# Optimization experiments

Measured on AMD Instinct MI355X. Metric: run time of the kernel, lower is better.

Reference implementation:

```python
import jax, jax.numpy as jnp
import numpy as np

TOP_K = 2


def setup_inputs() -> dict:
    key = jax.random.key(0)
    ks = jax.random.split(key, 6)
    B, S, H, I, E = 2, 1024, 1024, 2048, 8
    s_h = 1.0 / np.sqrt(H)
    s_i = 1.0 / np.sqrt(I)
    return {
        "x": jax.random.normal(ks[0], (B, S, H), jnp.float32),
        "gate_w": jax.random.normal(ks[1], (H, E), jnp.float32) * s_h,
        "gate_b": jnp.zeros((E,), jnp.float32),
        "w1": jax.random.normal(ks[2], (E, H, I), jnp.float32) * s_h,
        "w3": jax.random.normal(ks[3], (E, H, I), jnp.float32) * s_h,
        "w2": jax.random.normal(ks[4], (E, I, H), jnp.float32) * s_i,
    }


def reference(x, gate_w, gate_b, w1, w3, w2):
    # Gating: softmax over experts, then top-k selection + renormalization.
    logits = jnp.einsum("bsh,he->bse", x, gate_w) + gate_b            # [B,S,E]
    probs = jax.nn.softmax(logits, axis=-1)
    topk_w, topk_idx = jax.lax.top_k(probs, TOP_K)                    # [B,S,K]
    topk_w = topk_w / jnp.sum(topk_w, axis=-1, keepdims=True)

    E = gate_w.shape[-1]
    # Per-token combine weight for each expert (0 if not routed there).
    # one_hot: [B,S,K,E] -> combine: [B,S,E]
    combine = jnp.sum(jax.nn.one_hot(topk_idx, E, dtype=x.dtype) * topk_w[..., None], axis=-2)

    # SwiGLU expert FFN: down(silu(gate(x)) * up(x)); dense-masked reference
    # (compute every expert on every token, weight by combine; math identical
    # to the original gather/scatter loop since combine is 0 off-route).
    out = jnp.zeros_like(x)
    for e in range(E):
        h = jax.nn.silu(x @ w1[e]) * (x @ w3[e])                      # [B,S,I]
        out = out + combine[..., e:e + 1] * (h @ w2[e])               # [B,S,H]
    return out
```

## Files before the change

### kernel.cpp

```cpp
#include <hip/hip_runtime.h>
#include <hip/hip_bf16.h>
#include <math.h>

typedef __attribute__((ext_vector_type(4))) float f32x4;
typedef __attribute__((ext_vector_type(8))) short bf16x8;

#define T_TOK 2048
#define H_DIM 1024
#define I_DIM 2048
#define E_NUM 8

__device__ inline unsigned short f2bf(float f) {
  union { float f; unsigned int u; } v; v.f = f;
  unsigned int r = v.u + 0x7fffu + ((v.u >> 16) & 1u);
  return (unsigned short)(r >> 16);
}
__device__ inline unsigned int pack2(float a, float b) {
  return (unsigned int)f2bf(a) | ((unsigned int)f2bf(b) << 16);
}

__device__ inline void gld16(const void* g, void* l) {
  __builtin_amdgcn_global_load_lds((const __attribute__((address_space(1))) void*)g,
                                   (__attribute__((address_space(3))) void*)l, 16, 0, 0);
}

__device__ inline void transpose_tile(const float* __restrict__ ip, unsigned short* __restrict__ op,
                                      int R, int C, int rt, int ct, char* smem)
{
  unsigned short (*tl)[66] = (unsigned short (*)[66])smem;
  int r0 = rt * 64, c0 = ct * 64;
  int tid = threadIdx.x;
  int rq = (tid >> 4) * 4;
  int c4 = (tid & 15) * 4;
  const float* base = ip + (size_t)(r0 + rq) * C + c0 + c4;
  float4 v0 = *(const float4*)(base);
  float4 v1 = *(const float4*)(base + C);
  float4 v2 = *(const float4*)(base + 2 * C);
  float4 v3 = *(const float4*)(base + 3 * C);
  const float* f0 = (const float*)&v0;
  const float* f1 = (const float*)&v1;
  const float* f2 = (const float*)&v2;
  const float* f3 = (const float*)&v3;
#pragma unroll
  for (int j = 0; j < 4; ++j) {
    *(unsigned int*)&tl[c4 + j][rq]     = pack2(f0[j], f1[j]);
    *(unsigned int*)&tl[c4 + j][rq + 2] = pack2(f2[j], f3[j]);
  }
  __syncthreads();
  int c = tid >> 3, r8 = (tid & 7) * 8;
#pragma unroll
  for (int it = 0; it < 2; ++it) {
    int cc = c + it * 32;
    uint4 o;
    o.x = *(const unsigned int*)&tl[cc][r8];
    o.y = *(const unsigned int*)&tl[cc][r8 + 2];
    o.z = *(const unsigned int*)&tl[cc][r8 + 4];
    o.w = *(const unsigned int*)&tl[cc][r8 + 6];
    *(uint4*)(op + (size_t)(c0 + cc) * R + r0 + r8) = o;
  }
}

__global__ __launch_bounds__(256) void gate_t13(
    const float* __restrict__ x, const float* __restrict__ gw, const float* __restrict__ gb,
    int* __restrict__ rec_e, float* __restrict__ rec_w, unsigned short* __restrict__ xb,
    const float* __restrict__ w1, const float* __restrict__ w3,
    unsigned short* __restrict__ w1t, unsigned short* __restrict__ w3t)
{
  __shared__ __align__(16) char smem[64 * 66 * 2];
  int bx = blockIdx.x;
  if (bx >= 512) {
    int idx = bx - 512;
    int m = idx >> 9;
    int t9 = idx & 511;
    int rt = t9 & 15;
    int ct = t9 >> 4;
    const float* ip = (m < 8 ? w1 : w3) + (size_t)(m & 7) * ((size_t)H_DIM * I_DIM);
    unsigned short* op = (m < 8 ? w1t : w3t) + (size_t)(m & 7) * ((size_t)H_DIM * I_DIM);
    transpose_tile(ip, op, H_DIM, I_DIM, rt, ct, smem);
    return;
  }
  int wv = threadIdx.x >> 6, lane = threadIdx.x & 63;
  int t = bx * 4 + wv;
  const float* xr = x + (size_t)t * H_DIM;
  unsigned short* xo = xb + (size_t)t * H_DIM;
  float acc[8];
#pragma unroll
  for (int e = 0; e < 8; ++e) acc[e] = 0.f;
  for (int i = 0; i < H_DIM / 64; ++i) {
    int h = i * 64 + lane;
    float xv = xr[h];
    xo[h] = f2bf(xv);
    const float4* g = (const float4*)(gw + (size_t)h * 8);
    float4 g0 = g[0], g1 = g[1];
    acc[0] += xv * g0.x; acc[1] += xv * g0.y; acc[2] += xv * g0.z; acc[3] += xv * g0.w;
    acc[4] += xv * g1.x; acc[5] += xv * g1.y; acc[6] += xv * g1.z; acc[7] += xv * g1.w;
  }
#pragma unroll
  for (int s = 1; s < 64; s <<= 1) {
#pragma unroll
    for (int e = 0; e < 8; ++e) acc[e] += __shfl_xor(acc[e], s);
  }
  if (lane == 0) {
    float l[8];
#pragma unroll
    for (int e = 0; e < 8; ++e) l[e] = acc[e] + gb[e];
    int e0 = 0;
    for (int e = 1; e < 8; ++e) if (l[e] > l[e0]) e0 = e;
    int e1 = (e0 == 0) ? 1 : 0;
    for (int e = 0; e < 8; ++e) if (e != e0 && l[e] > l[e1]) e1 = e;
    float w0 = 1.f / (1.f + expf(l[e1] - l[e0]));
    rec_e[t * 2]     = e0; rec_e[t * 2 + 1] = e1;
    rec_w[t * 2]     = w0; rec_w[t * 2 + 1] = 1.f - w0;
  }
}

__global__ __launch_bounds__(256) void route8(
    const int* __restrict__ rec_e, const float* __restrict__ rec_w,
    int* __restrict__ counts_g, int* __restrict__ list_tok, float* __restrict__ list_w)
{
  __shared__ int cnt[8];
  __shared__ int fill;
  int e = blockIdx.x;
  int tid = threadIdx.x;
  if (tid < 8) cnt[tid] = 0;
  if (tid == 0) fill = 0;
  __syncthreads();
  int e_loc[16];
  int c_loc[8];
#pragma unroll
  for (int k = 0; k < 8; ++k) c_loc[k] = 0;
#pragma unroll
  for (int it = 0; it < 16; ++it) {
    e_loc[it] = rec_e[it * 256 + tid] & 7;
    c_loc[e_loc[it]]++;
  }
#pragma unroll
  for (int k = 0; k < 8; ++k) if (c_loc[k]) atomicAdd(&cnt[k], c_loc[k]);
  __syncthreads();
  if (e == 0 && tid < 8) counts_g[tid] = cnt[tid];
  int base = 0;
#pragma unroll
  for (int k = 0; k < 8; ++k) if (k < e) base += cnt[k];
#pragma unroll
  for (int it = 0; it < 16; ++it) {
    if (e_loc[it] == e) {
      int i = it * 256 + tid;
      int pos = atomicAdd(&fill, 1);
      list_tok[base + pos] = i;
      list_w[base + pos]   = rec_w[i];
    }
  }
}

__global__ __launch_bounds__(256, 2) void gemm1_t2(
    const unsigned short* __restrict__ xb,
    const unsigned short* __restrict__ w1t,
    const unsigned short* __restrict__ w3t,
    const int* __restrict__ counts,
    const int* __restrict__ list_tok,
    unsigned short* __restrict__ hbuf,
    const float* __restrict__ w2,
    unsigned short* __restrict__ w2t)
{
  __shared__ __align__(16) char smem[24576];
  int bx = blockIdx.x;
  if (bx >= 4096) {
    int idx = bx - 4096;
    int e = idx >> 9;
    int t9 = idx & 511;
    int rt = t9 & 31;
    int ct = t9 >> 5;
    const float* ip = w2 + (size_t)e * ((size_t)H_DIM * I_DIM);
    unsigned short* op = w2t + (size_t)e * ((size_t)H_DIM * I_DIM);
    transpose_tile(ip, op, I_DIM, H_DIM, rt, ct, smem);
    return;
  }
  int e = bx >> 9;
  int y = (bx >> 4) & 31;
  int ix = bx & 15;
  int nbase = 0;
#pragma unroll
  for (int i = 0; i < 8; ++i) if (i < e) nbase += counts[i];
  int n_e = counts[e];
  int t0 = y * 128;
  if (t0 >= n_e) return;
  int i0 = ix * 128;

  unsigned short* As  = (unsigned short*)smem;
  unsigned short* B1s = (unsigned short*)(smem + 8192);
  unsigned short* B3s = (unsigned short*)(smem + 16384);

  int tid = threadIdx.x;
  int r4 = tid >> 2;
  int seg = (tid & 3) * 8;

  int sr0 = t0 + r4;       if (sr0 >= n_e) sr0 = n_e - 1;
  int sr1 = t0 + 64 + r4;  if (sr1 >= n_e) sr1 = n_e - 1;
  int tok0 = list_tok[nbase + sr0] >> 1;
  int tok1 = list_tok[nbase + sr1] >> 1;
  const char* gA0 = (const char*)(xb + (size_t)tok0 * H_DIM + seg);
  const char* gA1 = (const char*)(xb + (size_t)tok1 * H_DIM + seg);
  const char* gB1a = (const char*)(w1t + ((size_t)e * I_DIM + i0 + r4) * H_DIM + seg);
  const char* gB1b = (const char*)(w1t + ((size_t)e * I_DIM + i0 + 64 + r4) * H_DIM + seg);
  const char* gB3a = (const char*)(w3t + ((size_t)e * I_DIM + i0 + r4) * H_DIM + seg);
  const char* gB3b = (const char*)(w3t + ((size_t)e * I_DIM + i0 + 64 + r4) * H_DIM + seg);

  char* lA0  = (char*)As + tid * 16;
  char* lA1  = (char*)As + 4096 + tid * 16;
  char* lB1a = (char*)B1s + tid * 16;
  char* lB1b = (char*)B1s + 4096 + tid * 16;
  char* lB3a = (char*)B3s + tid * 16;
  char* lB3b = (char*)B3s + 4096 + tid * 16;

  int w = tid >> 6, lane = tid & 63, lm = lane & 15, lq = lane >> 4;
  int wm = w & 1, wn = w >> 1;

  f32x4 acc1[4][4], acc3[4][4];
#pragma unroll
  for (int i = 0; i < 4; ++i)
#pragma unroll
    for (int j = 0; j < 4; ++j) { acc1[i][j] = (f32x4){0,0,0,0}; acc3[i][j] = (f32x4){0,0,0,0}; }

  for (int kb = 0; kb < H_DIM; kb += 32) {
    __syncthreads();
    gld16(gA0 + kb * 2, lA0);
    gld16(gA1 + kb * 2, lA1);
    gld16(gB1a + kb * 2, lB1a);
    gld16(gB1b + kb * 2, lB1b);
    gld16(gB3a + kb * 2, lB3a);
    gld16(gB3b + kb * 2, lB3b);
    __syncthreads();
    bf16x8 a[4], b1[4], b3[4];
#pragma unroll
    for (int i = 0; i < 4; ++i)
      a[i] = *(const bf16x8*)((const char*)As + 2 * ((wm * 64 + i * 16 + lm) * 32 + lq * 8));
#pragma unroll
    for (int j = 0; j < 4; ++j) {
      b1[j] = *(const bf16x8*)((const char*)B1s + 2 * ((wn * 64 + j * 16 + lm) * 32 + lq * 8));
      b3[j] = *(const bf16x8*)((const char*)B3s + 2 * ((wn * 64 + j * 16 + lm) * 32 + lq * 8));
    }
#pragma unroll
    for (int i = 0; i < 4; ++i)
#pragma unroll
      for (int j = 0; j < 4; ++j) {
        acc1[i][j] = __builtin_amdgcn_mfma_f32_16x16x32_bf16(a[i], b1[j], acc1[i][j], 0, 0, 0);
        acc3[i][j] = __builtin_amdgcn_mfma_f32_16x16x32_bf16(a[i], b3[j], acc3[i][j], 0, 0, 0);
      }
  }

#pragma unroll
  for (int i = 0; i < 4; ++i) {
#pragma unroll
    for (int rr = 0; rr < 4; ++rr) {
      int slot = t0 + wm * 64 + i * 16 + lq * 4 + rr;
      if (slot < n_e) {
        unsigned short* orow = hbuf + (size_t)(nbase + slot) * I_DIM + i0 + wn * 64 + lm;
#pragma unroll
        for (int j = 0; j < 4; ++j) {
          float g = acc1[i][j][rr], u = acc3[i][j][rr];
          float hv = (g / (1.f + __expf(-g))) * u;
          orow[j * 16] = f2bf(hv);
        }
      }
    }
  }
}

__global__ __launch_bounds__(256) void gemm2(
    const unsigned short* __restrict__ hbuf,
    const unsigned short* __restrict__ w2t,
    const int* __restrict__ counts,
    const int* __restrict__ list_tok,
    const float* __restrict__ list_w,
    float* __restrict__ partial)
{
  int e = blockIdx.z;
  int nbase = 0;
#pragma unroll
  for (int i = 0; i < 8; ++i) if (i < e) nbase += counts[i];
  int n_e = counts[e];
  int ts = blockIdx.y >> 2, kh = blockIdx.y & 3;
  int t0 = ts * 64;
  if (t0 >= n_e) return;
  int h0 = blockIdx.x * 128;
  int k0 = kh * (I_DIM / 4);

  __shared__ __align__(16) unsigned short As[64 * 32];
  __shared__ __align__(16) unsigned short Bs[128 * 32];

  int tid = threadIdx.x;
  int r = tid >> 2;
  int seg = (tid & 3) * 8;

  int sr = t0 + r; if (sr >= n_e) sr = n_e - 1;
  const char* gA  = (const char*)(hbuf + (size_t)(nbase + sr) * I_DIM + k0 + seg);
  const char* gB0 = (const char*)(w2t + ((size_t)e * H_DIM + h0 + r) * I_DIM + k0 + seg);
  const char* gB1 = (const char*)(w2t + ((size_t)e * H_DIM + h0 + 64 + r) * I_DIM + k0 + seg);

  char* lA  = (char*)As + tid * 16;
  char* lB0 = (char*)Bs + tid * 16;
  char* lB1 = (char*)Bs + 4096 + tid * 16;

  int w = tid >> 6, lane = tid & 63, lm = lane & 15, lq = lane >> 4;
  int wm = w & 1, wn = (w >> 1) * 64;

  f32x4 acc[2][4];
#pragma unroll
  for (int i = 0; i < 2; ++i)
#pragma unroll
    for (int j = 0; j < 4; ++j) acc[i][j] = (f32x4){0,0,0,0};

  for (int kb = 0; kb < I_DIM / 4; kb += 32) {
    __syncthreads();
    gld16(gA + kb * 2, lA);
    gld16(gB0 + kb * 2, lB0);
    gld16(gB1 + kb * 2, lB1);
    __syncthreads();
    bf16x8 a[2], b[4];
#pragma unroll
    for (int i = 0; i < 2; ++i)
      a[i] = *(const bf16x8*)((const char*)As + 2 * ((wm * 32 + i * 16 + lm) * 32 + lq * 8));
#pragma unroll
    for (int j = 0; j < 4; ++j)
      b[j] = *(const bf16x8*)((const char*)Bs + 2 * ((wn + j * 16 + lm) * 32 + lq * 8));
#pragma unroll
    for (int i = 0; i < 2; ++i)
#pragma unroll
      for (int j = 0; j < 4; ++j)
        acc[i][j] = __builtin_amdgcn_mfma_f32_16x16x32_bf16(a[i], b[j], acc[i][j], 0, 0, 0);
  }

  int entv[2][4]; float wtv[2][4];
#pragma unroll
  for (int i = 0; i < 2; ++i)
#pragma unroll
    for (int rr = 0; rr < 4; ++rr) {
      int slot = t0 + wm * 32 + i * 16 + lq * 4 + rr;
      if (slot < n_e) { entv[i][rr] = list_tok[nbase + slot]; wtv[i][rr] = list_w[nbase + slot]; }
      else entv[i][rr] = -1;
    }
#pragma unroll
  for (int i = 0; i < 2; ++i)
#pragma unroll
    for (int j = 0; j < 4; ++j)
#pragma unroll
      for (int rr = 0; rr < 4; ++rr) {
        if (entv[i][rr] >= 0) {
          int t = entv[i][rr] >> 1, kk = entv[i][rr] & 1;
          int plane = kh * 2 + kk;
          partial[((size_t)plane * T_TOK + t) * H_DIM + h0 + wn + j * 16 + lm] =
              acc[i][j][rr] * wtv[i][rr];
        }
      }
}

__global__ __launch_bounds__(256) void combine8(const float* __restrict__ partial,
                                                float* __restrict__ out)
{
  const size_t P = (size_t)T_TOK * H_DIM;
  size_t i = (size_t)(blockIdx.x * 256 + threadIdx.x) * 4;
  float4 s = *(const float4*)(partial + i);
#pragma unroll
  for (int p = 1; p < 8; ++p) {
    float4 v = *(const float4*)(partial + p * P + i);
    s.x += v.x; s.y += v.y; s.z += v.z; s.w += v.w;
  }
  *(float4*)(out + i) = s;
}

extern "C" void kernel_launch(void* const* d_in, const int* in_sizes, int n_in,
                              void* d_out, int out_size, void* d_ws, size_t ws_size,
                              hipStream_t stream) {
  const float* x  = (const float*)d_in[0];
  const float* gw = (const float*)d_in[1];
  const float* gb = (const float*)d_in[2];
  const float* w1 = (const float*)d_in[3];
  const float* w3 = (const float*)d_in[4];
  const float* w2 = (const float*)d_in[5];
  float* out = (float*)d_out;

  char* ws = (char*)d_ws;
  int*   counts   = (int*)(ws);
  int*   rec_e    = (int*)(ws + 128);
  float* rec_w    = (float*)(ws + 16512);
  int*   list_tok = (int*)(ws + 32896);
  float* list_w   = (float*)(ws + 49280);
  const size_t MB = 1024ull * 1024ull;
  unsigned short* xb   = (unsigned short*)(ws + 1 * MB);
  unsigned short* w1t  = (unsigned short*)(ws + 5 * MB);
  float* partial       = (float*)(ws + 5 * MB);
  unsigned short* w3t  = (unsigned short*)(ws + 37 * MB);
  unsigned short* w2t  = (unsigned short*)(ws + 69 * MB);
  unsigned short* hbuf = (unsigned short*)(ws + 101 * MB);

  gate_t13<<<512 + 8192, 256, 0, stream>>>(x, gw, gb, rec_e, rec_w, xb, w1, w3, w1t, w3t);
  route8<<<8, 256, 0, stream>>>(rec_e, rec_w, counts, list_tok, list_w);
  gemm1_t2<<<4096 + 4096, 256, 0, stream>>>(xb, w1t, w3t, counts, list_tok, hbuf, w2, w2t);
  gemm2<<<dim3(H_DIM / 128, 256, E_NUM), 256, 0, stream>>>(hbuf, w2t, counts, list_tok, list_w, partial);
  combine8<<<(T_TOK * H_DIM) / (256 * 4), 256, 0, stream>>>(partial, out);
}
```

Baseline: 348.0 us.

## Double K-step per GEMM iteration, halve gemm2 split-K, transpose two tiles per block

Both GEMMs now load a 64-wide K slice per barrier pair instead of 32, halving the number of syncs and making each block issue more loads before waiting. gemm2 drops its split-K from 4 to 2 partial planes, so the combine pass reads 4 planes instead of 8, and it gets a launch bound hint. The weight-transpose helper handles two row tiles per block, halving the number of transpose blocks. In exchange, LDS use per block doubles (48 KB in gemm1), which may lower occupancy, and gemm2 has fewer blocks with longer K loops.

```diff
diff --git a/kernel.cpp b/kernel.cpp
--- a/kernel.cpp
+++ b/kernel.cpp
@@ -24,39 +24,47 @@
                                    (__attribute__((address_space(3))) void*)l, 16, 0, 0);
 }
 
-__device__ inline void transpose_tile(const float* __restrict__ ip, unsigned short* __restrict__ op,
-                                      int R, int C, int rt, int ct, char* smem)
+__device__ inline void transpose_pair(const float* __restrict__ ip, unsigned short* __restrict__ op,
+                                      int R, int C, int rp, int ct, char* smem)
 {
   unsigned short (*tl)[66] = (unsigned short (*)[66])smem;
-  int r0 = rt * 64, c0 = ct * 64;
+  int r0 = rp * 128, c0 = ct * 64;
   int tid = threadIdx.x;
   int rq = (tid >> 4) * 4;
   int c4 = (tid & 15) * 4;
-  const float* base = ip + (size_t)(r0 + rq) * C + c0 + c4;
-  float4 v0 = *(const float4*)(base);
-  float4 v1 = *(const float4*)(base + C);
-  float4 v2 = *(const float4*)(base + 2 * C);
-  float4 v3 = *(const float4*)(base + 3 * C);
-  const float* f0 = (const float*)&v0;
-  const float* f1 = (const float*)&v1;
-  const float* f2 = (const float*)&v2;
-  const float* f3 = (const float*)&v3;
+  const float* b0 = ip + (size_t)(r0 + rq) * C + c0 + c4;
+  const float* b1 = b0 + (size_t)64 * C;
+  float4 v[8];
+  v[0] = *(const float4*)(b0);
+  v[1] = *(const float4*)(b0 + C);
+  v[2] = *(const float4*)(b0 + 2 * C);
+  v[3] = *(const float4*)(b0 + 3 * C);
+  v[4] = *(const float4*)(b1);
+  v[5] = *(const float4*)(b1 + C);
+  v[6] = *(const float4*)(b1 + 2 * C);
+  v[7] = *(const float4*)(b1 + 3 * C);
+  const float* f = (const float*)v;
 #pragma unroll
   for (int j = 0; j < 4; ++j) {
-    *(unsigned int*)&tl[c4 + j][rq]     = pack2(f0[j], f1[j]);
-    *(unsigned int*)&tl[c4 + j][rq + 2] = pack2(f2[j], f3[j]);
+    *(unsigned int*)&tl[c4 + j][rq]          = pack2(f[0 * 4 + j], f[1 * 4 + j]);
+    *(unsigned int*)&tl[c4 + j][rq + 2]      = pack2(f[2 * 4 + j], f[3 * 4 + j]);
+    *(unsigned int*)&tl[64 + c4 + j][rq]     = pack2(f[4 * 4 + j], f[5 * 4 + j]);
+    *(unsigned int*)&tl[64 + c4 + j][rq + 2] = pack2(f[6 * 4 + j], f[7 * 4 + j]);
   }
   __syncthreads();
   int c = tid >> 3, r8 = (tid & 7) * 8;
 #pragma unroll
   for (int it = 0; it < 2; ++it) {
     int cc = c + it * 32;
-    uint4 o;
-    o.x = *(const unsigned int*)&tl[cc][r8];
-    o.y = *(const unsigned int*)&tl[cc][r8 + 2];
-    o.z = *(const unsigned int*)&tl[cc][r8 + 4];
-    o.w = *(const unsigned int*)&tl[cc][r8 + 6];
-    *(uint4*)(op + (size_t)(c0 + cc) * R + r0 + r8) = o;
+#pragma unroll
+    for (int p = 0; p < 2; ++p) {
+      uint4 o;
+      o.x = *(const unsigned int*)&tl[p * 64 + cc][r8];
+      o.y = *(const unsigned int*)&tl[p * 64 + cc][r8 + 2];
+      o.z = *(const unsigned int*)&tl[p * 64 + cc][r8 + 4];
+      o.w = *(const unsigned int*)&tl[p * 64 + cc][r8 + 6];
+      *(uint4*)(op + (size_t)(c0 + cc) * R + r0 + p * 64 + r8) = o;
+    }
   }
 }
 
@@ -66,17 +74,17 @@
     const float* __restrict__ w1, const float* __restrict__ w3,
     unsigned short* __restrict__ w1t, unsigned short* __restrict__ w3t)
 {
-  __shared__ __align__(16) char smem[64 * 66 * 2];
+  __shared__ __align__(16) char smem[128 * 66 * 2];
   int bx = blockIdx.x;
   if (bx >= 512) {
     int idx = bx - 512;
-    int m = idx >> 9;
-    int t9 = idx & 511;
-    int rt = t9 & 15;
-    int ct = t9 >> 4;
+    int m = idx >> 8;
+    int t8 = idx & 255;
+    int rp = t8 & 7;
+    int ct = t8 >> 3;
     const float* ip = (m < 8 ? w1 : w3) + (size_t)(m & 7) * ((size_t)H_DIM * I_DIM);
     unsigned short* op = (m < 8 ? w1t : w3t) + (size_t)(m & 7) * ((size_t)H_DIM * I_DIM);
-    transpose_tile(ip, op, H_DIM, I_DIM, rt, ct, smem);
+    transpose_pair(ip, op, H_DIM, I_DIM, rp, ct, smem);
     return;
   }
   int wv = threadIdx.x >> 6, lane = threadIdx.x & 63;
@@ -162,17 +170,17 @@
     const float* __restrict__ w2,
     unsigned short* __restrict__ w2t)
 {
-  __shared__ __align__(16) char smem[24576];
+  __shared__ __align__(16) char smem[49152];
   int bx = blockIdx.x;
   if (bx >= 4096) {
     int idx = bx - 4096;
-    int e = idx >> 9;
-    int t9 = idx & 511;
-    int rt = t9 & 31;
-    int ct = t9 >> 5;
+    int e = idx >> 8;
+    int t8 = idx & 255;
+    int rp = t8 & 15;
+    int ct = t8 >> 4;
     const float* ip = w2 + (size_t)e * ((size_t)H_DIM * I_DIM);
     unsigned short* op = w2t + (size_t)e * ((size_t)H_DIM * I_DIM);
-    transpose_tile(ip, op, I_DIM, H_DIM, rt, ct, smem);
+    transpose_pair(ip, op, I_DIM, H_DIM, rp, ct, smem);
     return;
   }
   int e = bx >> 9;
@@ -186,31 +194,24 @@
   if (t0 >= n_e) return;
   int i0 = ix * 128;
 
-  unsigned short* As  = (unsigned short*)smem;
-  unsigned short* B1s = (unsigned short*)(smem + 8192);
-  unsigned short* B3s = (unsigned short*)(smem + 16384);
+  char* As  = smem;
+  char* B1s = smem + 16384;
+  char* B3s = smem + 32768;
 
   int tid = threadIdx.x;
-  int r4 = tid >> 2;
+  int r2 = tid >> 2;
   int seg = (tid & 3) * 8;
 
-  int sr0 = t0 + r4;       if (sr0 >= n_e) sr0 = n_e - 1;
-  int sr1 = t0 + 64 + r4;  if (sr1 >= n_e) sr1 = n_e - 1;
+  int sr0 = t0 + r2;       if (sr0 >= n_e) sr0 = n_e - 1;
+  int sr1 = t0 + 64 + r2;  if (sr1 >= n_e) sr1 = n_e - 1;
   int tok0 = list_tok[nbase + sr0] >> 1;
   int tok1 = list_tok[nbase + sr1] >> 1;
   const char* gA0 = (const char*)(xb + (size_t)tok0 * H_DIM + seg);
   const char* gA1 = (const char*)(xb + (size_t)tok1 * H_DIM + seg);
-  const char* gB1a = (const char*)(w1t + ((size_t)e * I_DIM + i0 + r4) * H_DIM + seg);
-  const char* gB1b = (const char*)(w1t + ((size_t)e * I_DIM + i0 + 64 + r4) * H_DIM + seg);
-  const char* gB3a = (const char*)(w3t + ((size_t)e * I_DIM + i0 + r4) * H_DIM + seg);
-  const char* gB3b = (const char*)(w3t + ((size_t)e * I_DIM + i0 + 64 + r4) * H_DIM + seg);
-
-  char* lA0  = (char*)As + tid * 16;
-  char* lA1  = (char*)As + 4096 + tid * 16;
-  char* lB1a = (char*)B1s + tid * 16;
-  char* lB1b = (char*)B1s + 4096 + tid * 16;
-  char* lB3a = (char*)B3s + tid * 16;
-  char* lB3b = (char*)B3s + 4096 + tid * 16;
+  const char* gB1a = (const char*)(w1t + ((size_t)e * I_DIM + i0 + r2) * H_DIM + seg);
+  const char* gB1b = (const char*)(w1t + ((size_t)e * I_DIM + i0 + 64 + r2) * H_DIM + seg);
+  const char* gB3a = (const char*)(w3t + ((size_t)e * I_DIM + i0 + r2) * H_DIM + seg);
+  const char* gB3b = (const char*)(w3t + ((size_t)e * I_DIM + i0 + 64 + r2) * H_DIM + seg);
 
   int w = tid >> 6, lane = tid & 63, lm = lane & 15, lq = lane >> 4;
   int wm = w & 1, wn = w >> 1;
@@ -221,31 +222,40 @@
 #pragma unroll
     for (int j = 0; j < 4; ++j) { acc1[i][j] = (f32x4){0,0,0,0}; acc3[i][j] = (f32x4){0,0,0,0}; }
 
-  for (int kb = 0; kb < H_DIM; kb += 32) {
+  for (int kb = 0; kb < H_DIM; kb += 64) {
     __syncthreads();
-    gld16(gA0 + kb * 2, lA0);
-    gld16(gA1 + kb * 2, lA1);
-    gld16(gB1a + kb * 2, lB1a);
-    gld16(gB1b + kb * 2, lB1b);
-    gld16(gB3a + kb * 2, lB3a);
-    gld16(gB3b + kb * 2, lB3b);
+    gld16(gA0 + kb * 2,       As + tid * 16);
+    gld16(gA1 + kb * 2,       As + 4096 + tid * 16);
+    gld16(gA0 + kb * 2 + 64,  As + 8192 + tid * 16);
+    gld16(gA1 + kb * 2 + 64,  As + 12288 + tid * 16);
+    gld16(gB1a + kb * 2,      B1s + tid * 16);
+    gld16(gB1b + kb * 2,      B1s + 4096 + tid * 16);
+    gld16(gB1a + kb * 2 + 64, B1s + 8192 + tid * 16);
+    gld16(gB1b + kb * 2 + 64, B1s + 12288 + tid * 16);
+    gld16(gB3a + kb * 2,      B3s + tid * 16);
+    gld16(gB3b + kb * 2,      B3s + 4096 + tid * 16);
+    gld16(gB3a + kb * 2 + 64, B3s + 8192 + tid * 16);
+    gld16(gB3b + kb * 2 + 64, B3s + 12288 + tid * 16);
     __syncthreads();
-    bf16x8 a[4], b1[4], b3[4];
-#pragma unroll
-    for (int i = 0; i < 4; ++i)
-      a[i] = *(const bf16x8*)((const char*)As + 2 * ((wm * 64 + i * 16 + lm) * 32 + lq * 8));
-#pragma unroll
-    for (int j = 0; j < 4; ++j) {
-      b1[j] = *(const bf16x8*)((const char*)B1s + 2 * ((wn * 64 + j * 16 + lm) * 32 + lq * 8));
-      b3[j] = *(const bf16x8*)((const char*)B3s + 2 * ((wn * 64 + j * 16 + lm) * 32 + lq * 8));
-    }
-#pragma unroll
-    for (int i = 0; i < 4; ++i)
+#pragma unroll
+    for (int s = 0; s < 2; ++s) {
+      bf16x8 a[4], b1[4], b3[4];
+#pragma unroll
+      for (int i = 0; i < 4; ++i)
+        a[i] = *(const bf16x8*)(As + s * 8192 + ((wm * 64 + i * 16 + lm) * 32 + lq * 8) * 2);
 #pragma unroll
       for (int j = 0; j < 4; ++j) {
-        acc1[i][j] = __builtin_amdgcn_mfma_f32_16x16x32_bf16(a[i], b1[j], acc1[i][j], 0, 0, 0);
-        acc3[i][j] = __builtin_amdgcn_mfma_f32_16x16x32_bf16(a[i], b3[j], acc3[i][j], 0, 0, 0);
+        b1[j] = *(const bf16x8*)(B1s + s * 8192 + ((wn * 64 + j * 16 + lm) * 32 + lq * 8) * 2);
+        b3[j] = *(const bf16x8*)(B3s + s * 8192 + ((wn * 64 + j * 16 + lm) * 32 + lq * 8) * 2);
       }
+#pragma unroll
+      for (int i = 0; i < 4; ++i)
+#pragma unroll
+        for (int j = 0; j < 4; ++j) {
+          acc1[i][j] = __builtin_amdgcn_mfma_f32_16x16x32_bf16(a[i], b1[j], acc1[i][j], 0, 0, 0);
+          acc3[i][j] = __builtin_amdgcn_mfma_f32_16x16x32_bf16(a[i], b3[j], acc3[i][j], 0, 0, 0);
+        }
+    }
   }
 
 #pragma unroll
@@ -266,7 +276,7 @@
   }
 }
 
-__global__ __launch_bounds__(256) void gemm2(
+__global__ __launch_bounds__(256, 4) void gemm2(
     const unsigned short* __restrict__ hbuf,
     const unsigned short* __restrict__ w2t,
     const int* __restrict__ counts,
@@ -274,32 +284,29 @@
     const float* __restrict__ list_w,
     float* __restrict__ partial)
 {
+  __shared__ __align__(16) char smem[24576];
   int e = blockIdx.z;
   int nbase = 0;
 #pragma unroll
   for (int i = 0; i < 8; ++i) if (i < e) nbase += counts[i];
   int n_e = counts[e];
-  int ts = blockIdx.y >> 2, kh = blockIdx.y & 3;
+  int ts = blockIdx.y >> 1, kh = blockIdx.y & 1;
   int t0 = ts * 64;
   if (t0 >= n_e) return;
   int h0 = blockIdx.x * 128;
-  int k0 = kh * (I_DIM / 4);
-
-  __shared__ __align__(16) unsigned short As[64 * 32];
-  __shared__ __align__(16) unsigned short Bs[128 * 32];
+  int k0 = kh * (I_DIM / 2);
+
+  char* As = smem;
+  char* Bs = smem + 8192;
 
   int tid = threadIdx.x;
-  int r = tid >> 2;
+  int r2 = tid >> 2;
   int seg = (tid & 3) * 8;
 
-  int sr = t0 + r; if (sr >= n_e) sr = n_e - 1;
+  int sr = t0 + r2; if (sr >= n_e) sr = n_e - 1;
   const char* gA  = (const char*)(hbuf + (size_t)(nbase + sr) * I_DIM + k0 + seg);
-  const char* gB0 = (const char*)(w2t + ((size_t)e * H_DIM + h0 + r) * I_DIM + k0 + seg);
-  const char* gB1 = (const char*)(w2t + ((size_t)e * H_DIM + h0 + 64 + r) * I_DIM + k0 + seg);
-
-  char* lA  = (char*)As + tid * 16;
-  char* lB0 = (char*)Bs + tid * 16;
-  char* lB1 = (char*)Bs + 4096 + tid * 16;
+  const char* gB0 = (const char*)(w2t + ((size_t)e * H_DIM + h0 + r2) * I_DIM + k0 + seg);
+  const char* gB1 = (const char*)(w2t + ((size_t)e * H_DIM + h0 + 64 + r2) * I_DIM + k0 + seg);
 
   int w = tid >> 6, lane = tid & 63, lm = lane & 15, lq = lane >> 4;
   int wm = w & 1, wn = (w >> 1) * 64;
@@ -310,24 +317,30 @@
 #pragma unroll
     for (int j = 0; j < 4; ++j) acc[i][j] = (f32x4){0,0,0,0};
 
-  for (int kb = 0; kb < I_DIM / 4; kb += 32) {
+  for (int kb = 0; kb < I_DIM / 2; kb += 64) {
     __syncthreads();
-    gld16(gA + kb * 2, lA);
-    gld16(gB0 + kb * 2, lB0);
-    gld16(gB1 + kb * 2, lB1);
+    gld16(gA + kb * 2,       As + tid * 16);
+    gld16(gA + kb * 2 + 64,  As + 4096 + tid * 16);
+    gld16(gB0 + kb * 2,      Bs + tid * 16);
+    gld16(gB1 + kb * 2,      Bs + 4096 + tid * 16);
+    gld16(gB0 + kb * 2 + 64, Bs + 8192 + tid * 16);
+    gld16(gB1 + kb * 2 + 64, Bs + 12288 + tid * 16);
     __syncthreads();
-    bf16x8 a[2], b[4];
-#pragma unroll
-    for (int i = 0; i < 2; ++i)
-      a[i] = *(const bf16x8*)((const char*)As + 2 * ((wm * 32 + i * 16 + lm) * 32 + lq * 8));
-#pragma unroll
-    for (int j = 0; j < 4; ++j)
-      b[j] = *(const bf16x8*)((const char*)Bs + 2 * ((wn + j * 16 + lm) * 32 + lq * 8));
-#pragma unroll
-    for (int i = 0; i < 2; ++i)
+#pragma unroll
+    for (int s = 0; s < 2; ++s) {
+      bf16x8 a[2], b[4];
+#pragma unroll
+      for (int i = 0; i < 2; ++i)
+        a[i] = *(const bf16x8*)(As + s * 4096 + ((wm * 32 + i * 16 + lm) * 32 + lq * 8) * 2);
 #pragma unroll
       for (int j = 0; j < 4; ++j)
-        acc[i][j] = __builtin_amdgcn_mfma_f32_16x16x32_bf16(a[i], b[j], acc[i][j], 0, 0, 0);
+        b[j] = *(const bf16x8*)(Bs + s * 8192 + ((wn + j * 16 + lm) * 32 + lq * 8) * 2);
+#pragma unroll
+      for (int i = 0; i < 2; ++i)
+#pragma unroll
+        for (int j = 0; j < 4; ++j)
+          acc[i][j] = __builtin_amdgcn_mfma_f32_16x16x32_bf16(a[i], b[j], acc[i][j], 0, 0, 0);
+    }
   }
 
   int entv[2][4]; float wtv[2][4];
@@ -354,18 +367,21 @@
       }
 }
 
-__global__ __launch_bounds__(256) void combine8(const float* __restrict__ partial,
+__global__ __launch_bounds__(256) void combine4(const float* __restrict__ partial,
                                                 float* __restrict__ out)
 {
   const size_t P = (size_t)T_TOK * H_DIM;
   size_t i = (size_t)(blockIdx.x * 256 + threadIdx.x) * 4;
-  float4 s = *(const float4*)(partial + i);
-#pragma unroll
-  for (int p = 1; p < 8; ++p) {
-    float4 v = *(const float4*)(partial + p * P + i);
-    s.x += v.x; s.y += v.y; s.z += v.z; s.w += v.w;
-  }
-  *(float4*)(out + i) = s;
+  float4 a = *(const float4*)(partial + i);
+  float4 b = *(const float4*)(partial + P + i);
+  float4 c = *(const float4*)(partial + 2 * P + i);
+  float4 d = *(const float4*)(partial + 3 * P + i);
+  float4 o;
+  o.x = a.x + b.x + c.x + d.x;
+  o.y = a.y + b.y + c.y + d.y;
+  o.z = a.z + b.z + c.z + d.z;
+  o.w = a.w + b.w + c.w + d.w;
+  *(float4*)(out + i) = o;
 }
 
 extern "C" void kernel_launch(void* const* d_in, const int* in_sizes, int n_in,
@@ -393,9 +409,9 @@
   unsigned short* w2t  = (unsigned short*)(ws + 69 * MB);
   unsigned short* hbuf = (unsigned short*)(ws + 101 * MB);
 
-  gate_t13<<<512 + 8192, 256, 0, stream>>>(x, gw, gb, rec_e, rec_w, xb, w1, w3, w1t, w3t);
+  gate_t13<<<512 + 4096, 256, 0, stream>>>(x, gw, gb, rec_e, rec_w, xb, w1, w3, w1t, w3t);
   route8<<<8, 256, 0, stream>>>(rec_e, rec_w, counts, list_tok, list_w);
-  gemm1_t2<<<4096 + 4096, 256, 0, stream>>>(xb, w1t, w3t, counts, list_tok, hbuf, w2, w2t);
-  gemm2<<<dim3(H_DIM / 128, 256, E_NUM), 256, 0, stream>>>(hbuf, w2t, counts, list_tok, list_w, partial);
-  combine8<<<(T_TOK * H_DIM) / (256 * 4), 256, 0, stream>>>(partial, out);
-}
+  gemm1_t2<<<4096 + 2048, 256, 0, stream>>>(xb, w1t, w3t, counts, list_tok, hbuf, w2, w2t);
+  gemm2<<<dim3(H_DIM / 128, 64, E_NUM), 256, 0, stream>>>(hbuf, w2t, counts, list_tok, list_w, partial);
+  combine4<<<(T_TOK * H_DIM) / (256 * 4), 256, 0, stream>>>(partial, out);
+}
```

New measurement: 336.6 us. 1.03x faster.
